# Kernel tuning notes

Hardware: AMD Instinct MI355X
Metric: run time of the kernel (lower is better)

The kernel has to match this reference:

```python
import jax, jax.numpy as jnp
import numpy as np

NUM_USERS = 100_000
NUM_ITEMS = 50_000
N_TOTAL = 150_100
EMBED_DIM = 64
NUM_LAYERS = 3
N_EDGES = 3_000_000
BATCH = 4096


def setup_inputs() -> dict:
    key = jax.random.key(0)
    k1, k2, k3, k4, k5, k6 = jax.random.split(key, 6)
    node_emb = jax.random.normal(k1, (N_TOTAL, EMBED_DIM), dtype=jnp.float32) * 0.1
    # COO sparse normalized adjacency (static irregular pattern)
    adj_row = jax.random.randint(k2, (N_EDGES,), 0, N_TOTAL, dtype=jnp.int32)
    adj_col = jax.random.randint(k3, (N_EDGES,), 0, N_TOTAL, dtype=jnp.int32)
    adj_val = jax.random.uniform(k4, (N_EDGES,), dtype=jnp.float32) * 0.05
    user_ids = jax.random.randint(k5, (BATCH,), 0, NUM_USERS, dtype=jnp.int32)
    item_ids = jax.random.randint(k6, (BATCH,), 0, NUM_ITEMS, dtype=jnp.int32)
    return {"node_emb": node_emb, "adj_val": adj_val, "adj_row": adj_row,
            "adj_col": adj_col, "user_ids": user_ids, "item_ids": item_ids}


def reference(node_emb, adj_val, adj_row, adj_col, user_ids, item_ids):
    # LightGCN propagation: K sparse SpMM layers, running mean over K+1 embeddings
    emb = node_emb                       # [N, D] layer-0
    acc = emb                            # running sum instead of stack+mean
    for _ in range(NUM_LAYERS):
        # SpMM: out[r] += val * emb[c]   (COO scatter-add)
        msgs = adj_val[:, None] * emb[adj_col]          # [E, D]
        emb = jax.ops.segment_sum(msgs, adj_row, num_segments=N_TOTAL)
        acc = acc + emb
    final = acc / jnp.float32(NUM_LAYERS + 1)           # mean over layers
    users = final[:NUM_USERS]
    items = final[NUM_USERS:NUM_USERS + NUM_ITEMS]
    u = users[user_ids]                                 # [B, D]
    i = items[item_ids]                                 # [B, D]
    return (u * i).sum(axis=-1)                         # [B]
```

## Files before the change

kernel.cpp:

```cpp
#include <hip/hip_runtime.h>

#define N_TOTAL    150100
#define NUM_USERS  100000
#define DIM        64
#define BSHIFT     8
#define BROWS      (1 << BSHIFT)
#define NBUK       ((N_TOTAL + BROWS - 1) / BROWS)
#define EPB        4096
#define CAP        5632
#define RSP        260

__device__ __forceinline__ unsigned bfr(float f) {
    unsigned u = __float_as_uint(f);
    return (u + 0x7FFFu + ((u >> 16) & 1u)) >> 16;
}
__device__ __forceinline__ unsigned pack2(float lo, float hi) {
    return bfr(lo) | (bfr(hi) << 16);
}
__device__ __forceinline__ float unlo(unsigned w) { return __uint_as_float(w << 16); }
__device__ __forceinline__ float unhi(unsigned w) { return __uint_as_float(w & 0xFFFF0000u); }

__global__ void convert_emb(const float4* __restrict__ in4,
                            uint2* __restrict__ outh, int n4,
                            int* __restrict__ gcount) {
    int t = blockIdx.x * blockDim.x + threadIdx.x;
    if (t < NBUK) gcount[t] = 0;
    if (t >= n4) return;
    float4 f = in4[t];
    outh[t] = make_uint2(pack2(f.x, f.y), pack2(f.z, f.w));
}

__global__ void __launch_bounds__(256) fill_buckets(
        const int* __restrict__ rows, const int* __restrict__ cols,
        const float* __restrict__ vals, int n_edges,
        int* __restrict__ gcount, int2* __restrict__ pair) {
    __shared__ int2  buf[EPB];
    __shared__ short tgtb[EPB];
    __shared__ int   hist[NBUK];
    __shared__ int   pref[NBUK];
    __shared__ int   loc[NBUK];
    __shared__ int   scan[256];
    const int tid = threadIdx.x;
    const int base = blockIdx.x * EPB;
    int end = base + EPB; if (end > n_edges) end = n_edges;
    const int cnt = end - base;

    for (int i = tid; i < NBUK; i += 256) hist[i] = 0;
    __syncthreads();
    for (int i = base + tid; i < end; i += 256)
        atomicAdd(&hist[rows[i] >> BSHIFT], 1);
    __syncthreads();
    const int t0 = tid * 3;
    int t1 = t0 + 3; if (t1 > NBUK) t1 = NBUK;
    int s = 0;
    for (int i = t0; i < t1; ++i) s += hist[i];
    scan[tid] = s;
    __syncthreads();
    for (int off = 1; off < 256; off <<= 1) {
        int v = 0;
        if (tid >= off) v = scan[tid - off];
        __syncthreads();
        if (tid >= off) scan[tid] += v;
        __syncthreads();
    }
    int run = (tid == 0) ? 0 : scan[tid - 1];
    for (int i = t0; i < t1; ++i) { int h = hist[i]; pref[i] = run; run += h; }
    __syncthreads();
    for (int b = tid; b < NBUK; b += 256) {
        int h = hist[b];
        loc[b] = h ? (b * CAP + atomicAdd(&gcount[b], h)) : 0;
        hist[b] = pref[b];
    }
    __syncthreads();
    for (int i = base + tid; i < end; i += 256) {
        int r = rows[i];
        int b = r >> BSHIFT;
        int pos = atomicAdd(&hist[b], 1);
        buf[pos] = make_int2(((r & (BROWS - 1)) << 18) | cols[i],
                             __float_as_int(vals[i]));
        tgtb[pos] = (short)b;
    }
    __syncthreads();
    for (int i = tid; i < cnt; i += 256) {
        int b = tgtb[i];
        int t = loc[b] + (i - pref[b]);
        if (t < NBUK * CAP)
            pair[t] = buf[i];
    }
}

__global__ void __launch_bounds__(256) bucket_sort(
        int2* __restrict__ pair,
        const int* __restrict__ gcount,
        int* __restrict__ rs) {
    __shared__ int2 buf[CAP];
    __shared__ int hist[BROWS];
    __shared__ int pref[BROWS];
    const int tid = threadIdx.x;
    const int b = blockIdx.x;
    const int k0 = b * CAP;
    int cnt = gcount[b]; if (cnt > CAP) cnt = CAP;

    hist[tid] = 0;
    __syncthreads();
    for (int i = tid; i < cnt; i += 256) {
        int2 e = pair[k0 + i];
        buf[i] = e;
        atomicAdd(&hist[e.x >> 18], 1);
    }
    __syncthreads();
    pref[tid] = hist[tid];
    __syncthreads();
    #pragma unroll
    for (int off = 1; off < BROWS; off <<= 1) {
        int v = 0;
        if (tid >= off) v = pref[tid - off];
        __syncthreads();
        if (tid >= off) pref[tid] += v;
        __syncthreads();
    }
    const int rbase = b << BSHIFT;
    int nrow = N_TOTAL - rbase; if (nrow > BROWS) nrow = BROWS;
    if (tid < nrow) {
        int ex = pref[tid] - hist[tid];
        rs[b * RSP + tid] = k0 + ex;
        hist[tid] = ex;
    }
    if (tid == 0) rs[b * RSP + nrow] = k0 + cnt;
    __syncthreads();
    for (int i = tid; i < cnt; i += 256) {
        int2 e = buf[i];
        int rl = e.x >> 18;
        int pos = atomicAdd(&hist[rl], 1);
        pair[k0 + pos] = make_int2(e.x & 0x3FFFF, e.y);
    }
}


#define SPMM_BODY(C, V)                                                        \
    do {                                                                       \
        uint2 w = embh[(size_t)(C) * 16 + sl];                                 \
        s.x += (V) * unlo(w.x); s.y += (V) * unhi(w.x);                        \
        s.z += (V) * unlo(w.y); s.w += (V) * unhi(w.y);                        \
    } while (0)

__global__ void spmm_bf16(const uint2* __restrict__ embh,
                          const int* __restrict__ rs,
                          const int2* __restrict__ pair,
                          uint2* __restrict__ outh) {
    int t = blockIdx.x * blockDim.x + threadIdx.x;
    int r = t >> 4;
    int sl = t & 15;
    int lane = threadIdx.x & 63;
    int subbase = lane & 48;
    if (r >= N_TOTAL) return;
    const int* rsb = rs + (r >> BSHIFT) * RSP + (r & (BROWS - 1));
    int k0 = rsb[0], k1 = rsb[1];
    float4 s = make_float4(0.f, 0.f, 0.f, 0.f);
    for (int kb = k0; kb < k1; kb += 16) {
        int cnt = k1 - kb; if (cnt > 16) cnt = 16;
        int2 pr = (sl < cnt) ? pair[kb + sl] : make_int2(0, 0);
        int j = 0;
        for (; j + 4 <= cnt; j += 4) {
            int   c0 = __shfl(pr.x, subbase + j + 0, 64);
            int   c1 = __shfl(pr.x, subbase + j + 1, 64);
            int   c2 = __shfl(pr.x, subbase + j + 2, 64);
            int   c3 = __shfl(pr.x, subbase + j + 3, 64);
            float v0 = __int_as_float(__shfl(pr.y, subbase + j + 0, 64));
            float v1 = __int_as_float(__shfl(pr.y, subbase + j + 1, 64));
            float v2 = __int_as_float(__shfl(pr.y, subbase + j + 2, 64));
            float v3 = __int_as_float(__shfl(pr.y, subbase + j + 3, 64));
            uint2 w0 = embh[(size_t)c0 * 16 + sl];
            uint2 w1 = embh[(size_t)c1 * 16 + sl];
            uint2 w2 = embh[(size_t)c2 * 16 + sl];
            uint2 w3 = embh[(size_t)c3 * 16 + sl];
            s.x += v0 * unlo(w0.x); s.y += v0 * unhi(w0.x);
            s.z += v0 * unlo(w0.y); s.w += v0 * unhi(w0.y);
            s.x += v1 * unlo(w1.x); s.y += v1 * unhi(w1.x);
            s.z += v1 * unlo(w1.y); s.w += v1 * unhi(w1.y);
            s.x += v2 * unlo(w2.x); s.y += v2 * unhi(w2.x);
            s.z += v2 * unlo(w2.y); s.w += v2 * unhi(w2.y);
            s.x += v3 * unlo(w3.x); s.y += v3 * unhi(w3.x);
            s.z += v3 * unlo(w3.y); s.w += v3 * unhi(w3.y);
        }
        for (; j < cnt; ++j) {
            int   c = __shfl(pr.x, subbase + j, 64);
            float v = __int_as_float(__shfl(pr.y, subbase + j, 64));
            SPMM_BODY(c, v);
        }
    }
    outh[(size_t)r * 16 + sl] = make_uint2(pack2(s.x, s.y), pack2(s.z, s.w));
}

__global__ void spmm_rows(const uint2* __restrict__ embh,
                          const int* __restrict__ rs,
                          const int2* __restrict__ pair,
                          const int* __restrict__ user_ids,
                          const int* __restrict__ item_ids,
                          float4* __restrict__ l3, int batch) {
    int t = blockIdx.x * blockDim.x + threadIdx.x;
    int b = t >> 4;
    int sl = t & 15;
    int lane = threadIdx.x & 63;
    int subbase = lane & 48;
    if (b >= 2 * batch) return;
    int r = (b < batch) ? user_ids[b] : (NUM_USERS + item_ids[b - batch]);
    const int* rsb = rs + (r >> BSHIFT) * RSP + (r & (BROWS - 1));
    int k0 = rsb[0], k1 = rsb[1];
    float4 s = make_float4(0.f, 0.f, 0.f, 0.f);
    for (int kb = k0; kb < k1; kb += 16) {
        int cnt = k1 - kb; if (cnt > 16) cnt = 16;
        int2 pr = (sl < cnt) ? pair[kb + sl] : make_int2(0, 0);
        for (int j = 0; j < cnt; ++j) {
            int   c = __shfl(pr.x, subbase + j, 64);
            float v = __int_as_float(__shfl(pr.y, subbase + j, 64));
            SPMM_BODY(c, v);
        }
    }
    l3[(size_t)b * 16 + sl] = s;
}

__global__ void final_dot_fused(const float4* __restrict__ emb4,
                                const uint2* __restrict__ A,
                                const uint2* __restrict__ B,
                                const float4* __restrict__ l3,
                                const int* __restrict__ user_ids,
                                const int* __restrict__ item_ids,
                                float* __restrict__ out, int batch) {
    int t = blockIdx.x * blockDim.x + threadIdx.x;
    int b = t >> 4, sl = t & 15;
    if (b >= batch) return;
    int u = user_ids[b];
    int iN = NUM_USERS + item_ids[b];

    float4 nu = emb4[(size_t)u * 16 + sl];
    uint2  au = A[(size_t)u * 16 + sl];
    uint2  bu = B[(size_t)u * 16 + sl];
    float4 lu = l3[(size_t)b * 16 + sl];
    float4 ni = emb4[(size_t)iN * 16 + sl];
    uint2  ai = A[(size_t)iN * 16 + sl];
    uint2  bi = B[(size_t)iN * 16 + sl];
    float4 li = l3[(size_t)(b + batch) * 16 + sl];

    float ux = nu.x + unlo(au.x) + unlo(bu.x) + lu.x;
    float uy = nu.y + unhi(au.x) + unhi(bu.x) + lu.y;
    float uz = nu.z + unlo(au.y) + unlo(bu.y) + lu.z;
    float uw = nu.w + unhi(au.y) + unhi(bu.y) + lu.w;
    float ix = ni.x + unlo(ai.x) + unlo(bi.x) + li.x;
    float iy = ni.y + unhi(ai.x) + unhi(bi.x) + li.y;
    float iz = ni.z + unlo(ai.y) + unlo(bi.y) + li.z;
    float iw = ni.w + unhi(ai.y) + unhi(bi.y) + li.w;

    float s = ux * ix + uy * iy + uz * iz + uw * iw;
    #pragma unroll
    for (int off = 8; off > 0; off >>= 1) s += __shfl_down(s, off, 64);
    if (sl == 0) out[b] = s * (1.0f / 16.0f);
}


static inline size_t align256(size_t x) { return (x + 255) & ~(size_t)255; }

extern "C" void kernel_launch(void* const* d_in, const int* in_sizes, int n_in,
                              void* d_out, int out_size, void* d_ws, size_t ws_size,
                              hipStream_t stream) {
    const float* node_emb = (const float*)d_in[0];
    const float* adj_val  = (const float*)d_in[1];
    const int*   adj_row  = (const int*)d_in[2];
    const int*   adj_col  = (const int*)d_in[3];
    const int*   user_ids = (const int*)d_in[4];
    const int*   item_ids = (const int*)d_in[5];
    float* out = (float*)d_out;

    const int n_edges = in_sizes[1];
    const int batch   = in_sizes[4];

    const size_t embh_bytes = (size_t)N_TOTAL * DIM * 2;

    char* p = (char*)d_ws;
    size_t off = 0;
    uint2* emb0h  = (uint2*)(p + off); off = align256(off + embh_bytes);
    uint2* bufAh  = (uint2*)(p + off); off = align256(off + embh_bytes);
    uint2* bufBh  = (uint2*)(p + off); off = align256(off + embh_bytes);
    float* l3buf  = (float*)(p + off); off = align256(off + (size_t)2 * batch * DIM * sizeof(float));
    int* gcount   = (int*)(p + off);   off = align256(off + (size_t)NBUK * sizeof(int));
    int* rs       = (int*)(p + off);   off = align256(off + (size_t)NBUK * RSP * sizeof(int));
    int2* pairA   = (int2*)(p + off);  off = align256(off + (size_t)NBUK * CAP * sizeof(int2));
    (void)ws_size;

    const int nbf = (n_edges + EPB - 1) / EPB;

    {
        int n4 = N_TOTAL * 16;
        convert_emb<<<(n4 + 255) / 256, 256, 0, stream>>>(
            (const float4*)node_emb, emb0h, n4, gcount);
    }

    fill_buckets<<<nbf, 256, 0, stream>>>(adj_row, adj_col, adj_val, n_edges,
                                          gcount, pairA);
    bucket_sort<<<NBUK, 256, 0, stream>>>(pairA, gcount, rs);

    const int rblocks = ((N_TOTAL * 16) + 255) / 256;
    const int gblocks = ((2 * batch * 16) + 255) / 256;

    spmm_bf16<<<rblocks, 256, 0, stream>>>(emb0h, rs, pairA, bufAh);
    spmm_bf16<<<rblocks, 256, 0, stream>>>(bufAh, rs, pairA, bufBh);
    spmm_rows<<<gblocks, 256, 0, stream>>>(bufBh, rs, pairA, user_ids,
                                           item_ids, (float4*)l3buf, batch);

    {
        int threads = batch * 16;
        final_dot_fused<<<(threads + 255) / 256, 256, 0, stream>>>(
            (const float4*)node_emb, bufAh, bufBh, (const float4*)l3buf,
            user_ids, item_ids, out, batch);
    }
}
```

Before: 310.4 us.

## Fuse layer-3 row SpMM into final dot and use wave-shuffle scans

```diff
diff --git a/kernel.cpp b/kernel.cpp
--- a/kernel.cpp
+++ b/kernel.cpp
@@ -20,6 +20,15 @@
 __device__ __forceinline__ float unlo(unsigned w) { return __uint_as_float(w << 16); }
 __device__ __forceinline__ float unhi(unsigned w) { return __uint_as_float(w & 0xFFFF0000u); }
 
+__device__ __forceinline__ int wave_incl_scan(int x, int lane) {
+    #pragma unroll
+    for (int off = 1; off < 64; off <<= 1) {
+        int y = __shfl_up(x, off, 64);
+        if (lane >= off) x += y;
+    }
+    return x;
+}
+
 __global__ void convert_emb(const float4* __restrict__ in4,
                             uint2* __restrict__ outh, int n4,
                             int* __restrict__ gcount) {
@@ -38,9 +47,11 @@
     __shared__ short tgtb[EPB];
     __shared__ int   hist[NBUK];
     __shared__ int   pref[NBUK];
+    __shared__ int   cur[NBUK];
     __shared__ int   loc[NBUK];
-    __shared__ int   scan[256];
+    __shared__ int   wtot[4];
     const int tid = threadIdx.x;
+    const int lane = tid & 63, wid = tid >> 6;
     const int base = blockIdx.x * EPB;
     int end = base + EPB; if (end > n_edges) end = n_edges;
     const int cnt = end - base;
@@ -50,32 +61,31 @@
     for (int i = base + tid; i < end; i += 256)
         atomicAdd(&hist[rows[i] >> BSHIFT], 1);
     __syncthreads();
+    for (int b = tid; b < NBUK; b += 256) {
+        int h = hist[b];
+        loc[b] = h ? atomicAdd(&gcount[b], h) : 0;
+    }
     const int t0 = tid * 3;
     int t1 = t0 + 3; if (t1 > NBUK) t1 = NBUK;
     int s = 0;
     for (int i = t0; i < t1; ++i) s += hist[i];
-    scan[tid] = s;
-    __syncthreads();
-    for (int off = 1; off < 256; off <<= 1) {
-        int v = 0;
-        if (tid >= off) v = scan[tid - off];
-        __syncthreads();
-        if (tid >= off) scan[tid] += v;
-        __syncthreads();
-    }
-    int run = (tid == 0) ? 0 : scan[tid - 1];
-    for (int i = t0; i < t1; ++i) { int h = hist[i]; pref[i] = run; run += h; }
-    __syncthreads();
-    for (int b = tid; b < NBUK; b += 256) {
-        int h = hist[b];
-        loc[b] = h ? (b * CAP + atomicAdd(&gcount[b], h)) : 0;
-        hist[b] = pref[b];
+    int incl = wave_incl_scan(s, lane);
+    if (lane == 63) wtot[wid] = incl;
+    __syncthreads();
+    int wofs = 0;
+    for (int w = 0; w < wid; ++w) wofs += wtot[w];
+    int run = incl + wofs - s;
+    for (int i = t0; i < t1; ++i) {
+        int h = hist[i];
+        pref[i] = run;
+        cur[i] = run;
+        run += h;
     }
     __syncthreads();
     for (int i = base + tid; i < end; i += 256) {
         int r = rows[i];
         int b = r >> BSHIFT;
-        int pos = atomicAdd(&hist[b], 1);
+        int pos = atomicAdd(&cur[b], 1);
         buf[pos] = make_int2(((r & (BROWS - 1)) << 18) | cols[i],
                              __float_as_int(vals[i]));
         tgtb[pos] = (short)b;
@@ -83,9 +93,9 @@
     __syncthreads();
     for (int i = tid; i < cnt; i += 256) {
         int b = tgtb[i];
-        int t = loc[b] + (i - pref[b]);
-        if (t < NBUK * CAP)
-            pair[t] = buf[i];
+        int o = loc[b] + (i - pref[b]);
+        if (o < CAP)
+            pair[b * CAP + o] = buf[i];
     }
 }
 
@@ -95,8 +105,10 @@
         int* __restrict__ rs) {
     __shared__ int2 buf[CAP];
     __shared__ int hist[BROWS];
-    __shared__ int pref[BROWS];
+    __shared__ int curl[BROWS];
+    __shared__ int wtot[4];
     const int tid = threadIdx.x;
+    const int lane = tid & 63, wid = tid >> 6;
     const int b = blockIdx.x;
     const int k0 = b * CAP;
     int cnt = gcount[b]; if (cnt > CAP) cnt = CAP;
@@ -109,29 +121,23 @@
         atomicAdd(&hist[e.x >> 18], 1);
     }
     __syncthreads();
-    pref[tid] = hist[tid];
-    __syncthreads();
-    #pragma unroll
-    for (int off = 1; off < BROWS; off <<= 1) {
-        int v = 0;
-        if (tid >= off) v = pref[tid - off];
-        __syncthreads();
-        if (tid >= off) pref[tid] += v;
-        __syncthreads();
-    }
+    int s = hist[tid];
+    int incl = wave_incl_scan(s, lane);
+    if (lane == 63) wtot[wid] = incl;
+    __syncthreads();
+    int wofs = 0;
+    for (int w = 0; w < wid; ++w) wofs += wtot[w];
+    int ex = incl + wofs - s;
     const int rbase = b << BSHIFT;
     int nrow = N_TOTAL - rbase; if (nrow > BROWS) nrow = BROWS;
-    if (tid < nrow) {
-        int ex = pref[tid] - hist[tid];
-        rs[b * RSP + tid] = k0 + ex;
-        hist[tid] = ex;
-    }
+    if (tid < nrow) rs[b * RSP + tid] = k0 + ex;
     if (tid == 0) rs[b * RSP + nrow] = k0 + cnt;
+    curl[tid] = ex;
     __syncthreads();
     for (int i = tid; i < cnt; i += 256) {
         int2 e = buf[i];
         int rl = e.x >> 18;
-        int pos = atomicAdd(&hist[rl], 1);
+        int pos = atomicAdd(&curl[rl], 1);
         pair[k0 + pos] = make_int2(e.x & 0x3FFFF, e.y);
     }
 }
@@ -192,19 +198,10 @@
     outh[(size_t)r * 16 + sl] = make_uint2(pack2(s.x, s.y), pack2(s.z, s.w));
 }
 
-__global__ void spmm_rows(const uint2* __restrict__ embh,
-                          const int* __restrict__ rs,
-                          const int2* __restrict__ pair,
-                          const int* __restrict__ user_ids,
-                          const int* __restrict__ item_ids,
-                          float4* __restrict__ l3, int batch) {
-    int t = blockIdx.x * blockDim.x + threadIdx.x;
-    int b = t >> 4;
-    int sl = t & 15;
-    int lane = threadIdx.x & 63;
-    int subbase = lane & 48;
-    if (b >= 2 * batch) return;
-    int r = (b < batch) ? user_ids[b] : (NUM_USERS + item_ids[b - batch]);
+__device__ __forceinline__ float4 rowsum_bf16(const uint2* __restrict__ embh,
+                                              const int* __restrict__ rs,
+                                              const int2* __restrict__ pair,
+                                              int r, int sl, int subbase) {
     const int* rsb = rs + (r >> BSHIFT) * RSP + (r & (BROWS - 1));
     int k0 = rsb[0], k1 = rsb[1];
     float4 s = make_float4(0.f, 0.f, 0.f, 0.f);
@@ -214,33 +211,39 @@
         for (int j = 0; j < cnt; ++j) {
             int   c = __shfl(pr.x, subbase + j, 64);
             float v = __int_as_float(__shfl(pr.y, subbase + j, 64));
-            SPMM_BODY(c, v);
+            uint2 w = embh[(size_t)c * 16 + sl];
+            s.x += v * unlo(w.x); s.y += v * unhi(w.x);
+            s.z += v * unlo(w.y); s.w += v * unhi(w.y);
         }
     }
-    l3[(size_t)b * 16 + sl] = s;
+    return s;
 }
 
 __global__ void final_dot_fused(const float4* __restrict__ emb4,
                                 const uint2* __restrict__ A,
                                 const uint2* __restrict__ B,
-                                const float4* __restrict__ l3,
+                                const int* __restrict__ rs,
+                                const int2* __restrict__ pair,
                                 const int* __restrict__ user_ids,
                                 const int* __restrict__ item_ids,
                                 float* __restrict__ out, int batch) {
     int t = blockIdx.x * blockDim.x + threadIdx.x;
     int b = t >> 4, sl = t & 15;
+    int lane = threadIdx.x & 63;
+    int subbase = lane & 48;
     if (b >= batch) return;
     int u = user_ids[b];
     int iN = NUM_USERS + item_ids[b];
 
+    float4 lu = rowsum_bf16(B, rs, pair, u, sl, subbase);
+    float4 li = rowsum_bf16(B, rs, pair, iN, sl, subbase);
+
     float4 nu = emb4[(size_t)u * 16 + sl];
     uint2  au = A[(size_t)u * 16 + sl];
     uint2  bu = B[(size_t)u * 16 + sl];
-    float4 lu = l3[(size_t)b * 16 + sl];
     float4 ni = emb4[(size_t)iN * 16 + sl];
     uint2  ai = A[(size_t)iN * 16 + sl];
     uint2  bi = B[(size_t)iN * 16 + sl];
-    float4 li = l3[(size_t)(b + batch) * 16 + sl];
 
     float ux = nu.x + unlo(au.x) + unlo(bu.x) + lu.x;
     float uy = nu.y + unhi(au.x) + unhi(bu.x) + lu.y;
@@ -281,7 +284,6 @@
     uint2* emb0h  = (uint2*)(p + off); off = align256(off + embh_bytes);
     uint2* bufAh  = (uint2*)(p + off); off = align256(off + embh_bytes);
     uint2* bufBh  = (uint2*)(p + off); off = align256(off + embh_bytes);
-    float* l3buf  = (float*)(p + off); off = align256(off + (size_t)2 * batch * DIM * sizeof(float));
     int* gcount   = (int*)(p + off);   off = align256(off + (size_t)NBUK * sizeof(int));
     int* rs       = (int*)(p + off);   off = align256(off + (size_t)NBUK * RSP * sizeof(int));
     int2* pairA   = (int2*)(p + off);  off = align256(off + (size_t)NBUK * CAP * sizeof(int2));
@@ -300,17 +302,14 @@
     bucket_sort<<<NBUK, 256, 0, stream>>>(pairA, gcount, rs);
 
     const int rblocks = ((N_TOTAL * 16) + 255) / 256;
-    const int gblocks = ((2 * batch * 16) + 255) / 256;
 
     spmm_bf16<<<rblocks, 256, 0, stream>>>(emb0h, rs, pairA, bufAh);
     spmm_bf16<<<rblocks, 256, 0, stream>>>(bufAh, rs, pairA, bufBh);
-    spmm_rows<<<gblocks, 256, 0, stream>>>(bufBh, rs, pairA, user_ids,
-                                           item_ids, (float4*)l3buf, batch);
 
     {
         int threads = batch * 16;
         final_dot_fused<<<(threads + 255) / 256, 256, 0, stream>>>(
-            (const float4*)node_emb, bufAh, bufBh, (const float4*)l3buf,
+            (const float4*)node_emb, bufAh, bufBh, rs, pairA,
             user_ids, item_ids, out, batch);
     }
 }
```

After: 315.6 us. Within noise of the previous version (+1.7%).
